# Performance work log

Hardware: AMD Instinct MI355X
Metric: run time of the kernel (lower is better)

## Reference

```python
import jax, jax.numpy as jnp
import numpy as np

N, K, D = 32768, 32, 64
LOG_2PI = float(np.log(2.0 * np.pi))


def setup_inputs() -> dict:
    key = jax.random.key(0)
    k1, k2, k3, k4 = jax.random.split(key, 4)
    X = jax.random.normal(k1, (N, D), dtype=jnp.float32)
    mu = jax.random.normal(k2, (K, D), dtype=jnp.float32)
    L = jax.random.normal(k3, (K, D, D), dtype=jnp.float32) * 0.1
    weights = jax.random.normal(k4, (K,), dtype=jnp.float32)
    return {"X": X, "mu": mu, "L": L, "weights": weights, "it": 0}


def reference(X, mu, L, weights, it):
    d = X.shape[1]
    # Cholesky composition: Sigma_k = tril(L_k) @ tril(L_k).T + I  (always PD)
    Lt = jnp.tril(L)                                   # [K, D, D]
    sigmas = Lt @ jnp.swapaxes(Lt, -1, -2) + jnp.eye(d, dtype=X.dtype)
    _, logdet = jnp.linalg.slogdet(sigmas)             # [K] (det > 0, sign = +1)
    Sinv = jnp.linalg.inv(sigmas)                      # [K, D, D]
    # Batched squared Mahalanobis distance: [N, K]
    diff = X[:, None, :] - mu[None, :, :]              # [N, K, D]
    maha = jnp.einsum("nkd,kde,nke->nk", diff, Sinv, diff)
    log_w = jax.nn.log_softmax(weights)                # [K]
    # log component density + log mixture weight
    logp = -0.5 * (d * LOG_2PI + logdet[None, :] + maha) + log_w[None, :]
    # pdf = sum_k exp(logp); log_likelihood = log(pdf)  (stable via logsumexp)
    loglik = jax.scipy.special.logsumexp(logp, axis=1)  # [N]
    # forward = -log_likelihoods(X).logsumexp(dim=0)
    return -jax.scipy.special.logsumexp(loglik, axis=0)
```

## Files before the change

kernel.cpp:

```cpp
#include <hip/hip_runtime.h>
#include <math.h>

#define DIM 64
#define KC 32
#define NPTS 32768
#define LOG_2PI 1.8378770664093453f
#define C0 (-58.0f)
#define ST 68

typedef __attribute__((ext_vector_type(8))) short short8;
typedef __attribute__((ext_vector_type(4))) float float4v;

__device__ __forceinline__ unsigned short f2bf(float f) {
    unsigned u = __float_as_uint(f);
    u += 0x7FFFu + ((u >> 16) & 1u);
    return (unsigned short)(u >> 16);
}

__device__ __forceinline__ float rdlane(float v, int l) {
    return __int_as_float(__builtin_amdgcn_readlane(__float_as_int(v), l));
}

__global__ __launch_bounds__(256) void conv_kernel(
    const float* __restrict__ X, short* __restrict__ Xbf)
{
    const int ctid = blockIdx.x * 256 + threadIdx.x;
    const float4* xin = (const float4*)X + (size_t)ctid * 2;
    float4 v0 = xin[0], v1 = xin[1];
    short8 o;
    o[0] = (short)f2bf(v0.x); o[1] = (short)f2bf(v0.y);
    o[2] = (short)f2bf(v0.z); o[3] = (short)f2bf(v0.w);
    o[4] = (short)f2bf(v1.x); o[5] = (short)f2bf(v1.y);
    o[6] = (short)f2bf(v1.z); o[7] = (short)f2bf(v1.w);
    *((short8*)Xbf + ctid) = o;
}

__global__ __launch_bounds__(256) void prep_kernel(
    const float* __restrict__ L, const float* __restrict__ mu,
    const float* __restrict__ w, short* __restrict__ Bpack,
    float* __restrict__ qpackN, float* __restrict__ cstC)
{
    const int k = blockIdx.x;
    const int t = threadIdx.x;
    const int wv = t >> 6;
    const int ln = t & 63;
    __shared__ float Llds[DIM * ST];
    __shared__ float Sig[DIM * ST];
    __shared__ float Clds[DIM * ST];
    __shared__ float Ylds[DIM * ST];
    __shared__ float rdbuf[DIM];

    for (int idx = t; idx < DIM * DIM; idx += 256) {
        int r = idx >> 6, c = idx & 63;
        float v = L[(size_t)k * DIM * DIM + idx];
        Llds[r * ST + c] = (c <= r) ? v : 0.f;
    }
    for (int idx = t; idx < DIM * ST; idx += 256) {
        Clds[idx] = 0.f;
        Ylds[idx] = 0.f;
    }
    __syncthreads();

    {
        float Lr[DIM];
        const float4* lp = (const float4*)(Llds + ln * ST);
#pragma unroll
        for (int p = 0; p < 16; ++p) {
            float4 v = lp[p];
            Lr[4 * p] = v.x; Lr[4 * p + 1] = v.y;
            Lr[4 * p + 2] = v.z; Lr[4 * p + 3] = v.w;
        }
#pragma unroll
        for (int jj = 0; jj < 16; ++jj) {
            const int j = jj * 4 + wv;
            const float4* up = (const float4*)(Llds + j * ST);
            const int pc = jj + 1;
            float a0 = 0.f, a1 = 0.f, a2 = 0.f, a3 = 0.f;
#pragma unroll
            for (int p = 0; p < pc; ++p) {
                float4 u = up[p];
                a0 = fmaf(Lr[4 * p], u.x, a0);
                a1 = fmaf(Lr[4 * p + 1], u.y, a1);
                a2 = fmaf(Lr[4 * p + 2], u.z, a2);
                a3 = fmaf(Lr[4 * p + 3], u.w, a3);
            }
            float s = (a0 + a1) + (a2 + a3);
            if (j == ln) s += 1.f;
            Sig[ln * ST + j] = s;
        }
    }
    __syncthreads();

    float ld2 = 0.f;
    {
        float Cr[DIM];
        float Yr[DIM];
#pragma unroll
        for (int c = 0; c < DIM; c += 8) {
            const float4* u0 = (const float4*)(Clds + (c + 0) * ST);
            const float4* u1 = (const float4*)(Clds + (c + 1) * ST);
            const float4* u2 = (const float4*)(Clds + (c + 2) * ST);
            const float4* u3 = (const float4*)(Clds + (c + 3) * ST);
            const float4* u4 = (const float4*)(Clds + (c + 4) * ST);
            const float4* u5 = (const float4*)(Clds + (c + 5) * ST);
            const float4* u6 = (const float4*)(Clds + (c + 6) * ST);
            const float4* u7 = (const float4*)(Clds + (c + 7) * ST);
            const int pc = c >> 2;
            float si0 = 0.f, si1 = 0.f, si2 = 0.f, si3 = 0.f;
            float si4 = 0.f, si5 = 0.f, si6 = 0.f, si7 = 0.f;
            if (wv == 0) {
                float d0a = 0.f, d0b = 0.f, d1a = 0.f, d1b = 0.f;
                float d2a = 0.f, d2b = 0.f, d3a = 0.f, d3b = 0.f;
                float d4a = 0.f, d4b = 0.f, d5a = 0.f, d5b = 0.f;
                float d6a = 0.f, d6b = 0.f, d7a = 0.f, d7b = 0.f;
#pragma unroll
                for (int p = 0; p < pc; ++p) {
                    float crx = Cr[4 * p], cry = Cr[4 * p + 1];
                    float crz = Cr[4 * p + 2], crw = Cr[4 * p + 3];
                    float4 q0 = u0[p], q1 = u1[p], q2 = u2[p], q3 = u3[p];
                    float4 q4 = u4[p], q5 = u5[p], q6 = u6[p], q7 = u7[p];
                    d0a = fmaf(crx, q0.x, d0a); d0b = fmaf(cry, q0.y, d0b);
                    d0a = fmaf(crz, q0.z, d0a); d0b = fmaf(crw, q0.w, d0b);
                    d1a = fmaf(crx, q1.x, d1a); d1b = fmaf(cry, q1.y, d1b);
                    d1a = fmaf(crz, q1.z, d1a); d1b = fmaf(crw, q1.w, d1b);
                    d2a = fmaf(crx, q2.x, d2a); d2b = fmaf(cry, q2.y, d2b);
                    d2a = fmaf(crz, q2.z, d2a); d2b = fmaf(crw, q2.w, d2b);
                    d3a = fmaf(crx, q3.x, d3a); d3b = fmaf(cry, q3.y, d3b);
                    d3a = fmaf(crz, q3.z, d3a); d3b = fmaf(crw, q3.w, d3b);
                    d4a = fmaf(crx, q4.x, d4a); d4b = fmaf(cry, q4.y, d4b);
                    d4a = fmaf(crz, q4.z, d4a); d4b = fmaf(crw, q4.w, d4b);
                    d5a = fmaf(crx, q5.x, d5a); d5b = fmaf(cry, q5.y, d5b);
                    d5a = fmaf(crz, q5.z, d5a); d5b = fmaf(crw, q5.w, d5b);
                    d6a = fmaf(crx, q6.x, d6a); d6b = fmaf(cry, q6.y, d6b);
                    d6a = fmaf(crz, q6.z, d6a); d6b = fmaf(crw, q6.w, d6b);
                    d7a = fmaf(crx, q7.x, d7a); d7b = fmaf(cry, q7.y, d7b);
                    d7a = fmaf(crz, q7.z, d7a); d7b = fmaf(crw, q7.w, d7b);
                }
                const float4 sgA = *(const float4*)(Sig + ln * ST + c);
                const float4 sgB = *(const float4*)(Sig + ln * ST + c + 4);
                float s0 = sgA.x - (d0a + d0b);
                float s1 = sgA.y - (d1a + d1b);
                float s2 = sgA.z - (d2a + d2b);
                float s3 = sgA.w - (d3a + d3b);
                float s4 = sgB.x - (d4a + d4b);
                float s5 = sgB.y - (d5a + d5b);
                float s6 = sgB.z - (d6a + d6b);
                float s7 = sgB.w - (d7a + d7b);
                float dd0 = rdlane(s0, c + 0);
                float rd0 = __builtin_amdgcn_rsqf(dd0);
                float c0v = s0 * rd0;
                s1 = fmaf(-c0v, rdlane(c0v, c + 1), s1);
                s2 = fmaf(-c0v, rdlane(c0v, c + 2), s2);
                s3 = fmaf(-c0v, rdlane(c0v, c + 3), s3);
                s4 = fmaf(-c0v, rdlane(c0v, c + 4), s4);
                s5 = fmaf(-c0v, rdlane(c0v, c + 5), s5);
                s6 = fmaf(-c0v, rdlane(c0v, c + 6), s6);
                s7 = fmaf(-c0v, rdlane(c0v, c + 7), s7);
                float dd1 = rdlane(s1, c + 1);
                float rd1 = __builtin_amdgcn_rsqf(dd1);
                float c1v = s1 * rd1;
                s2 = fmaf(-c1v, rdlane(c1v, c + 2), s2);
                s3 = fmaf(-c1v, rdlane(c1v, c + 3), s3);
                s4 = fmaf(-c1v, rdlane(c1v, c + 4), s4);
                s5 = fmaf(-c1v, rdlane(c1v, c + 5), s5);
                s6 = fmaf(-c1v, rdlane(c1v, c + 6), s6);
                s7 = fmaf(-c1v, rdlane(c1v, c + 7), s7);
                float dd2 = rdlane(s2, c + 2);
                float rd2 = __builtin_amdgcn_rsqf(dd2);
                float c2v = s2 * rd2;
                s3 = fmaf(-c2v, rdlane(c2v, c + 3), s3);
                s4 = fmaf(-c2v, rdlane(c2v, c + 4), s4);
                s5 = fmaf(-c2v, rdlane(c2v, c + 5), s5);
                s6 = fmaf(-c2v, rdlane(c2v, c + 6), s6);
                s7 = fmaf(-c2v, rdlane(c2v, c + 7), s7);
                float dd3 = rdlane(s3, c + 3);
                float rd3 = __builtin_amdgcn_rsqf(dd3);
                float c3v = s3 * rd3;
                s4 = fmaf(-c3v, rdlane(c3v, c + 4), s4);
                s5 = fmaf(-c3v, rdlane(c3v, c + 5), s5);
                s6 = fmaf(-c3v, rdlane(c3v, c + 6), s6);
                s7 = fmaf(-c3v, rdlane(c3v, c + 7), s7);
                float dd4 = rdlane(s4, c + 4);
                float rd4 = __builtin_amdgcn_rsqf(dd4);
                float c4v = s4 * rd4;
                s5 = fmaf(-c4v, rdlane(c4v, c + 5), s5);
                s6 = fmaf(-c4v, rdlane(c4v, c + 6), s6);
                s7 = fmaf(-c4v, rdlane(c4v, c + 7), s7);
                float dd5 = rdlane(s5, c + 5);
                float rd5 = __builtin_amdgcn_rsqf(dd5);
                float c5v = s5 * rd5;
                s6 = fmaf(-c5v, rdlane(c5v, c + 6), s6);
                s7 = fmaf(-c5v, rdlane(c5v, c + 7), s7);
                float dd6 = rdlane(s6, c + 6);
                float rd6 = __builtin_amdgcn_rsqf(dd6);
                float c6v = s6 * rd6;
                s7 = fmaf(-c6v, rdlane(c6v, c + 7), s7);
                float dd7 = rdlane(s7, c + 7);
                float rd7 = __builtin_amdgcn_rsqf(dd7);
                float c7v = s7 * rd7;
                ld2 += ((__logf(dd0) + __logf(dd1)) + (__logf(dd2) + __logf(dd3)))
                     + ((__logf(dd4) + __logf(dd5)) + (__logf(dd6) + __logf(dd7)));
                Cr[c + 0] = c0v; Cr[c + 1] = c1v; Cr[c + 2] = c2v; Cr[c + 3] = c3v;
                Cr[c + 4] = c4v; Cr[c + 5] = c5v; Cr[c + 6] = c6v; Cr[c + 7] = c7v;
                *(float4*)(Clds + ln * ST + c)     = make_float4(c0v, c1v, c2v, c3v);
                *(float4*)(Clds + ln * ST + c + 4) = make_float4(c4v, c5v, c6v, c7v);
                if (ln == 0) {
                    *(float4*)(rdbuf + c)     = make_float4(rd0, rd1, rd2, rd3);
                    *(float4*)(rdbuf + c + 4) = make_float4(rd4, rd5, rd6, rd7);
                }
            } else if (wv == 1) {
                float e0a = 0.f, e0b = 0.f, e1a = 0.f, e1b = 0.f;
                float e2a = 0.f, e2b = 0.f, e3a = 0.f, e3b = 0.f;
                float e4a = 0.f, e4b = 0.f, e5a = 0.f, e5b = 0.f;
                float e6a = 0.f, e6b = 0.f, e7a = 0.f, e7b = 0.f;
#pragma unroll
                for (int p = 0; p < pc; ++p) {
                    float yrx = Yr[4 * p], yry = Yr[4 * p + 1];
                    float yrz = Yr[4 * p + 2], yrw = Yr[4 * p + 3];
                    float4 q0 = u0[p], q1 = u1[p], q2 = u2[p], q3 = u3[p];
                    float4 q4 = u4[p], q5 = u5[p], q6 = u6[p], q7 = u7[p];
                    e0a = fmaf(yrx, q0.x, e0a); e0b = fmaf(yry, q0.y, e0b);
                    e0a = fmaf(yrz, q0.z, e0a); e0b = fmaf(yrw, q0.w, e0b);
                    e1a = fmaf(yrx, q1.x, e1a); e1b = fmaf(yry, q1.y, e1b);
                    e1a = fmaf(yrz, q1.z, e1a); e1b = fmaf(yrw, q1.w, e1b);
                    e2a = fmaf(yrx, q2.x, e2a); e2b = fmaf(yry, q2.y, e2b);
                    e2a = fmaf(yrz, q2.z, e2a); e2b = fmaf(yrw, q2.w, e2b);
                    e3a = fmaf(yrx, q3.x, e3a); e3b = fmaf(yry, q3.y, e3b);
                    e3a = fmaf(yrz, q3.z, e3a); e3b = fmaf(yrw, q3.w, e3b);
                    e4a = fmaf(yrx, q4.x, e4a); e4b = fmaf(yry, q4.y, e4b);
                    e4a = fmaf(yrz, q4.z, e4a); e4b = fmaf(yrw, q4.w, e4b);
                    e5a = fmaf(yrx, q5.x, e5a); e5b = fmaf(yry, q5.y, e5b);
                    e5a = fmaf(yrz, q5.z, e5a); e5b = fmaf(yrw, q5.w, e5b);
                    e6a = fmaf(yrx, q6.x, e6a); e6b = fmaf(yry, q6.y, e6b);
                    e6a = fmaf(yrz, q6.z, e6a); e6b = fmaf(yrw, q6.w, e6b);
                    e7a = fmaf(yrx, q7.x, e7a); e7b = fmaf(yry, q7.y, e7b);
                    e7a = fmaf(yrz, q7.z, e7a); e7b = fmaf(yrw, q7.w, e7b);
                }
                si0 = ((ln == c + 0) ? 1.f : 0.f) - (e0a + e0b);
                si1 = ((ln == c + 1) ? 1.f : 0.f) - (e1a + e1b);
                si2 = ((ln == c + 2) ? 1.f : 0.f) - (e2a + e2b);
                si3 = ((ln == c + 3) ? 1.f : 0.f) - (e3a + e3b);
                si4 = ((ln == c + 4) ? 1.f : 0.f) - (e4a + e4b);
                si5 = ((ln == c + 5) ? 1.f : 0.f) - (e5a + e5b);
                si6 = ((ln == c + 6) ? 1.f : 0.f) - (e6a + e6b);
                si7 = ((ln == c + 7) ? 1.f : 0.f) - (e7a + e7b);
            }
            __syncthreads();
            if (wv == 1) {
                const float4 rdv0 = *(const float4*)(rdbuf + c);
                const float4 rdv1 = *(const float4*)(rdbuf + c + 4);
                const float4 r1  = *(const float4*)(Clds + (c + 1) * ST + c);
                const float4 r2  = *(const float4*)(Clds + (c + 2) * ST + c);
                const float4 r3  = *(const float4*)(Clds + (c + 3) * ST + c);
                const float4 r4  = *(const float4*)(Clds + (c + 4) * ST + c);
                const float4 r5a = *(const float4*)(Clds + (c + 5) * ST + c);
                const float4 r5b = *(const float4*)(Clds + (c + 5) * ST + c + 4);
                const float4 r6a = *(const float4*)(Clds + (c + 6) * ST + c);
                const float4 r6b = *(const float4*)(Clds + (c + 6) * ST + c + 4);
                const float4 r7a = *(const float4*)(Clds + (c + 7) * ST + c);
                const float4 r7b = *(const float4*)(Clds + (c + 7) * ST + c + 4);
                float y0 = si0 * rdv0.x;
                float y1 = (si1 - r1.x * y0) * rdv0.y;
                float y2 = (si2 - r2.x * y0 - r2.y * y1) * rdv0.z;
                float y3 = (si3 - r3.x * y0 - r3.y * y1 - r3.z * y2) * rdv0.w;
                float y4 = (si4 - r4.x * y0 - r4.y * y1 - r4.z * y2 - r4.w * y3) * rdv1.x;
                float y5 = (si5 - r5a.x * y0 - r5a.y * y1 - r5a.z * y2 - r5a.w * y3
                                - r5b.x * y4) * rdv1.y;
                float y6 = (si6 - r6a.x * y0 - r6a.y * y1 - r6a.z * y2 - r6a.w * y3
                                - r6b.x * y4 - r6b.y * y5) * rdv1.z;
                float y7 = (si7 - r7a.x * y0 - r7a.y * y1 - r7a.z * y2 - r7a.w * y3
                                - r7b.x * y4 - r7b.y * y5 - r7b.z * y6) * rdv1.w;
                float4 yo0, yo1;
                yo0.x = (ln <= c + 0) ? y0 : 0.f;
                yo0.y = (ln <= c + 1) ? y1 : 0.f;
                yo0.z = (ln <= c + 2) ? y2 : 0.f;
                yo0.w = (ln <= c + 3) ? y3 : 0.f;
                yo1.x = (ln <= c + 4) ? y4 : 0.f;
                yo1.y = (ln <= c + 5) ? y5 : 0.f;
                yo1.z = (ln <= c + 6) ? y6 : 0.f;
                yo1.w = (ln <= c + 7) ? y7 : 0.f;
                Yr[c + 0] = yo0.x; Yr[c + 1] = yo0.y;
                Yr[c + 2] = yo0.z; Yr[c + 3] = yo0.w;
                Yr[c + 4] = yo1.x; Yr[c + 5] = yo1.y;
                Yr[c + 6] = yo1.z; Yr[c + 7] = yo1.w;
                *(float4*)(Ylds + ln * ST + c)     = yo0;
                *(float4*)(Ylds + ln * ST + c + 4) = yo1;
            }
        }
    }
    __syncthreads();

    if (wv == 0) {
        const float* muk = mu + k * DIM;
        float qv = 0.f;
#pragma unroll 8
        for (int j = 0; j < DIM; ++j)
            qv = fmaf(Ylds[j * ST + ln], muk[j], qv);
        qpackN[k * DIM + ln] = -qv;
        float wl = (ln < KC) ? w[ln] : -3.0e38f;
        float wm = wl;
#pragma unroll
        for (int m = 1; m <= 32; m <<= 1)
            wm = fmaxf(wm, __shfl_xor(wm, m, 64));
        float ex = (ln < KC) ? __expf(wl - wm) : 0.f;
#pragma unroll
        for (int m = 1; m <= 32; m <<= 1)
            ex += __shfl_xor(ex, m, 64);
        if (ln == 0) {
            float logw = w[k] - (wm + __logf(ex));
            cstC[k] = -0.5f * (DIM * LOG_2PI + ld2) + logw - C0;
        }
    }
    __syncthreads();

    {
        const int ct = wv;
        const int col = ct * 16 + (ln & 15);
        const int kb = (ln >> 4) * 8;
#pragma unroll
        for (int kt = 0; kt < 2; ++kt) {
            short8 v;
#pragma unroll
            for (int e = 0; e < 8; ++e)
                v[e] = (short)f2bf(Ylds[(kt * 32 + kb + e) * ST + col]);
            *(short8*)(Bpack + ((size_t)(k * 8 + ct * 2 + kt) * 64 + ln) * 8) = v;
        }
    }
}

__global__ __launch_bounds__(256, 4) void main_kernel(
    const short* __restrict__ Xbf, const float* __restrict__ Bpack,
    const float* __restrict__ qpackN, const float* __restrict__ cstC,
    float* __restrict__ partials)
{
    const int tid = threadIdx.x;
    const int lane = tid & 63;
    const int wv = tid >> 6;
    const int ks = blockIdx.x & 7;
    const int g = blockIdx.x >> 3;

    __shared__ float4 Bsh[2048];
    __shared__ float qsh[256];
    {
        const float4* Bg = (const float4*)Bpack + (size_t)ks * 2048;
#pragma unroll
        for (int it = 0; it < 8; ++it)
            Bsh[it * 256 + tid] = Bg[it * 256 + tid];
        qsh[tid] = qpackN[ks * 256 + tid];
    }

    const int rbase = g * 128 + wv * 32;
    const int jb = (lane >> 4) * 8;
    const int j8 = jb >> 3;
    const short8* xr = (const short8*)Xbf + (size_t)(rbase + (lane & 15)) * 8;
    short8 a0  = xr[j8];
    short8 a1  = xr[j8 + 4];
    short8 b0r = xr[j8 + 128];
    short8 b1r = xr[j8 + 132];

    __syncthreads();

    const short8* Bs = (const short8*)Bsh;
    float acc = 0.f;
#pragma unroll
    for (int kk = 0; kk < 4; ++kk) {
        const int k = ks * 4 + kk;
        float pA = 0.f, pB = 0.f;
#pragma unroll
        for (int ct = 0; ct < 4; ++ct) {
            short8 f0 = Bs[(kk * 8 + ct * 2 + 0) * 64 + lane];
            short8 f1 = Bs[(kk * 8 + ct * 2 + 1) * 64 + lane];
            const float4 nq4 = *(const float4*)(qsh + kk * 64 + ct * 16 + (lane >> 4) * 4);
            float4v c0 = {nq4.x, nq4.y, nq4.z, nq4.w};
            c0 = __builtin_amdgcn_mfma_f32_16x16x32_bf16(f0, a0, c0, 0, 0, 0);
            c0 = __builtin_amdgcn_mfma_f32_16x16x32_bf16(f1, a1, c0, 0, 0, 0);
            float4v c1 = {nq4.x, nq4.y, nq4.z, nq4.w};
            c1 = __builtin_amdgcn_mfma_f32_16x16x32_bf16(f0, b0r, c1, 0, 0, 0);
            c1 = __builtin_amdgcn_mfma_f32_16x16x32_bf16(f1, b1r, c1, 0, 0, 0);
            pA = fmaf(c0[0], c0[0], pA); pA = fmaf(c0[1], c0[1], pA);
            pA = fmaf(c0[2], c0[2], pA); pA = fmaf(c0[3], c0[3], pA);
            pB = fmaf(c1[0], c1[0], pB); pB = fmaf(c1[1], c1[1], pB);
            pB = fmaf(c1[2], c1[2], pB); pB = fmaf(c1[3], c1[3], pB);
        }
        pA += __shfl_xor(pA, 16, 64);
        pA += __shfl_xor(pA, 32, 64);
        pB += __shfl_xor(pB, 16, 64);
        pB += __shfl_xor(pB, 32, 64);
        const float cc = cstC[k];
        acc += __expf(fmaf(-0.5f, pA, cc)) + __expf(fmaf(-0.5f, pB, cc));
    }
    acc += __shfl_xor(acc, 1, 64);
    acc += __shfl_xor(acc, 2, 64);
    acc += __shfl_xor(acc, 4, 64);
    acc += __shfl_xor(acc, 8, 64);

    __shared__ float pm[4];
    if (lane == 0) pm[wv] = acc;
    __syncthreads();
    if (tid == 0)
        partials[blockIdx.x] = (pm[0] + pm[1]) + (pm[2] + pm[3]);
}

__global__ __launch_bounds__(256) void final_kernel(
    const float* __restrict__ partials, int n, float* __restrict__ out)
{
    const int tid = threadIdx.x;
    float s = 0.f;
    for (int i = tid; i < n; i += 256) s += partials[i];
#pragma unroll
    for (int m = 1; m <= 32; m <<= 1) s += __shfl_xor(s, m, 64);
    __shared__ float pm[4];
    if ((tid & 63) == 0) pm[tid >> 6] = s;
    __syncthreads();
    if (tid == 0) out[0] = -(C0 + logf((pm[0] + pm[1]) + (pm[2] + pm[3])));
}

extern "C" void kernel_launch(void* const* d_in, const int* in_sizes, int n_in,
                              void* d_out, int out_size, void* d_ws, size_t ws_size,
                              hipStream_t stream) {
    const float* X  = (const float*)d_in[0];
    const float* mu = (const float*)d_in[1];
    const float* L  = (const float*)d_in[2];
    const float* w  = (const float*)d_in[3];

    char* ws = (char*)d_ws;
    short* Bpack  = (short*)ws;
    float* qpackN = (float*)(ws + (256 << 10));
    float* cstC   = qpackN + KC * DIM;
    float* parts  = cstC + KC;
    short* Xbf    = (short*)(ws + (4 << 20));

    conv_kernel<<<1024, 256, 0, stream>>>(X, Xbf);
    prep_kernel<<<KC, 256, 0, stream>>>(L, mu, w, Bpack, qpackN, cstC);
    main_kernel<<<2048, 256, 0, stream>>>(Xbf, (const float*)Bpack, qpackN, cstC, parts);
    final_kernel<<<1, 256, 0, stream>>>(parts, 2048, (float*)d_out);
}
```

Measured before the change: 99.91 us.

## Fuse final reduction into main kernel via atomics and halve block count

Removes the separate final_kernel launch. Each main_kernel block now atomically adds its partial sum and increments a counter, and the last block to arrive computes the log and writes the output. The accumulator and counter are zeroed in conv_kernel. Each block also processes two row tiles, so the grid drops from 2048 to 1024 blocks and the B-tile LDS load is amortised over twice as many rows. The trade-off is a float atomic sum whose order varies between runs, so the result is non-deterministic, and fewer blocks means less parallelism.

```diff
diff --git a/kernel.cpp b/kernel.cpp
--- a/kernel.cpp
+++ b/kernel.cpp
@@ -22,8 +22,13 @@
 }
 
 __global__ __launch_bounds__(256) void conv_kernel(
-    const float* __restrict__ X, short* __restrict__ Xbf)
+    const float* __restrict__ X, short* __restrict__ Xbf,
+    float* __restrict__ accum, unsigned* __restrict__ counter)
 {
+    if (blockIdx.x == 0 && threadIdx.x == 0) {
+        *accum = 0.f;
+        *counter = 0u;
+    }
     const int ctid = blockIdx.x * 256 + threadIdx.x;
     const float4* xin = (const float4*)X + (size_t)ctid * 2;
     float4 v0 = xin[0], v1 = xin[1];
@@ -331,7 +336,8 @@
 __global__ __launch_bounds__(256, 4) void main_kernel(
     const short* __restrict__ Xbf, const float* __restrict__ Bpack,
     const float* __restrict__ qpackN, const float* __restrict__ cstC,
-    float* __restrict__ partials)
+    float* __restrict__ accum, unsigned* __restrict__ counter,
+    float* __restrict__ out)
 {
     const int tid = threadIdx.x;
     const int lane = tid & 63;
@@ -348,46 +354,47 @@
             Bsh[it * 256 + tid] = Bg[it * 256 + tid];
         qsh[tid] = qpackN[ks * 256 + tid];
     }
-
-    const int rbase = g * 128 + wv * 32;
-    const int jb = (lane >> 4) * 8;
-    const int j8 = jb >> 3;
-    const short8* xr = (const short8*)Xbf + (size_t)(rbase + (lane & 15)) * 8;
-    short8 a0  = xr[j8];
-    short8 a1  = xr[j8 + 4];
-    short8 b0r = xr[j8 + 128];
-    short8 b1r = xr[j8 + 132];
+    const int j8 = lane >> 4;
 
     __syncthreads();
 
     const short8* Bs = (const short8*)Bsh;
     float acc = 0.f;
-#pragma unroll
-    for (int kk = 0; kk < 4; ++kk) {
-        const int k = ks * 4 + kk;
-        float pA = 0.f, pB = 0.f;
-#pragma unroll
-        for (int ct = 0; ct < 4; ++ct) {
-            short8 f0 = Bs[(kk * 8 + ct * 2 + 0) * 64 + lane];
-            short8 f1 = Bs[(kk * 8 + ct * 2 + 1) * 64 + lane];
-            const float4 nq4 = *(const float4*)(qsh + kk * 64 + ct * 16 + (lane >> 4) * 4);
-            float4v c0 = {nq4.x, nq4.y, nq4.z, nq4.w};
-            c0 = __builtin_amdgcn_mfma_f32_16x16x32_bf16(f0, a0, c0, 0, 0, 0);
-            c0 = __builtin_amdgcn_mfma_f32_16x16x32_bf16(f1, a1, c0, 0, 0, 0);
-            float4v c1 = {nq4.x, nq4.y, nq4.z, nq4.w};
-            c1 = __builtin_amdgcn_mfma_f32_16x16x32_bf16(f0, b0r, c1, 0, 0, 0);
-            c1 = __builtin_amdgcn_mfma_f32_16x16x32_bf16(f1, b1r, c1, 0, 0, 0);
-            pA = fmaf(c0[0], c0[0], pA); pA = fmaf(c0[1], c0[1], pA);
-            pA = fmaf(c0[2], c0[2], pA); pA = fmaf(c0[3], c0[3], pA);
-            pB = fmaf(c1[0], c1[0], pB); pB = fmaf(c1[1], c1[1], pB);
-            pB = fmaf(c1[2], c1[2], pB); pB = fmaf(c1[3], c1[3], pB);
-        }
-        pA += __shfl_xor(pA, 16, 64);
-        pA += __shfl_xor(pA, 32, 64);
-        pB += __shfl_xor(pB, 16, 64);
-        pB += __shfl_xor(pB, 32, 64);
-        const float cc = cstC[k];
-        acc += __expf(fmaf(-0.5f, pA, cc)) + __expf(fmaf(-0.5f, pB, cc));
+#pragma unroll 1
+    for (int rr = 0; rr < 2; ++rr) {
+        const int rbase = g * 256 + rr * 128 + wv * 32;
+        const short8* xr = (const short8*)Xbf + (size_t)(rbase + (lane & 15)) * 8;
+        short8 a0  = xr[j8];
+        short8 a1  = xr[j8 + 4];
+        short8 b0r = xr[j8 + 128];
+        short8 b1r = xr[j8 + 132];
+#pragma unroll
+        for (int kk = 0; kk < 4; ++kk) {
+            const int k = ks * 4 + kk;
+            float pA = 0.f, pB = 0.f;
+#pragma unroll
+            for (int ct = 0; ct < 4; ++ct) {
+                short8 f0 = Bs[(kk * 8 + ct * 2 + 0) * 64 + lane];
+                short8 f1 = Bs[(kk * 8 + ct * 2 + 1) * 64 + lane];
+                const float4 nq4 = *(const float4*)(qsh + kk * 64 + ct * 16 + j8 * 4);
+                float4v c0 = {nq4.x, nq4.y, nq4.z, nq4.w};
+                c0 = __builtin_amdgcn_mfma_f32_16x16x32_bf16(f0, a0, c0, 0, 0, 0);
+                c0 = __builtin_amdgcn_mfma_f32_16x16x32_bf16(f1, a1, c0, 0, 0, 0);
+                float4v c1 = {nq4.x, nq4.y, nq4.z, nq4.w};
+                c1 = __builtin_amdgcn_mfma_f32_16x16x32_bf16(f0, b0r, c1, 0, 0, 0);
+                c1 = __builtin_amdgcn_mfma_f32_16x16x32_bf16(f1, b1r, c1, 0, 0, 0);
+                pA = fmaf(c0[0], c0[0], pA); pA = fmaf(c0[1], c0[1], pA);
+                pA = fmaf(c0[2], c0[2], pA); pA = fmaf(c0[3], c0[3], pA);
+                pB = fmaf(c1[0], c1[0], pB); pB = fmaf(c1[1], c1[1], pB);
+                pB = fmaf(c1[2], c1[2], pB); pB = fmaf(c1[3], c1[3], pB);
+            }
+            pA += __shfl_xor(pA, 16, 64);
+            pA += __shfl_xor(pA, 32, 64);
+            pB += __shfl_xor(pB, 16, 64);
+            pB += __shfl_xor(pB, 32, 64);
+            const float cc = cstC[k];
+            acc += __expf(fmaf(-0.5f, pA, cc)) + __expf(fmaf(-0.5f, pB, cc));
+        }
     }
     acc += __shfl_xor(acc, 1, 64);
     acc += __shfl_xor(acc, 2, 64);
@@ -397,22 +404,17 @@
     __shared__ float pm[4];
     if (lane == 0) pm[wv] = acc;
     __syncthreads();
-    if (tid == 0)
-        partials[blockIdx.x] = (pm[0] + pm[1]) + (pm[2] + pm[3]);
-}
-
-__global__ __launch_bounds__(256) void final_kernel(
-    const float* __restrict__ partials, int n, float* __restrict__ out)
-{
-    const int tid = threadIdx.x;
-    float s = 0.f;
-    for (int i = tid; i < n; i += 256) s += partials[i];
-#pragma unroll
-    for (int m = 1; m <= 32; m <<= 1) s += __shfl_xor(s, m, 64);
-    __shared__ float pm[4];
-    if ((tid & 63) == 0) pm[tid >> 6] = s;
-    __syncthreads();
-    if (tid == 0) out[0] = -(C0 + logf((pm[0] + pm[1]) + (pm[2] + pm[3])));
+    if (tid == 0) {
+        const float part = (pm[0] + pm[1]) + (pm[2] + pm[3]);
+        atomicAdd(accum, part);
+        __threadfence();
+        const unsigned old = atomicAdd(counter, 1u);
+        if (old == 1023u) {
+            __threadfence();
+            const float s = atomicAdd(accum, 0.f);
+            out[0] = -(C0 + __logf(s) );
+        }
+    }
 }
 
 extern "C" void kernel_launch(void* const* d_in, const int* in_sizes, int n_in,
@@ -427,11 +429,12 @@
     short* Bpack  = (short*)ws;
     float* qpackN = (float*)(ws + (256 << 10));
     float* cstC   = qpackN + KC * DIM;
-    float* parts  = cstC + KC;
+    float* accum  = cstC + KC;
+    unsigned* counter = (unsigned*)(accum + 1);
     short* Xbf    = (short*)(ws + (4 << 20));
 
-    conv_kernel<<<1024, 256, 0, stream>>>(X, Xbf);
+    conv_kernel<<<1024, 256, 0, stream>>>(X, Xbf, accum, counter);
     prep_kernel<<<KC, 256, 0, stream>>>(L, mu, w, Bpack, qpackN, cstC);
-    main_kernel<<<2048, 256, 0, stream>>>(Xbf, (const float*)Bpack, qpackN, cstC, parts);
-    final_kernel<<<1, 256, 0, stream>>>(parts, 2048, (float*)d_out);
-}
+    main_kernel<<<1024, 256, 0, stream>>>(Xbf, (const float*)Bpack, qpackN, cstC,
+                                          accum, counter, (float*)d_out);
+}
```

Measured after the change: 172.5 us. +72.6%, slower.

## Compute Sigma columns lazily inside the Cholesky loop on idle waves

Applied to the files above, without the earlier changes.

Instead of building the full Sigma = L L^T + I matrix before the factorisation, waves 2-3 compute only the first 8 columns up front. The remaining columns are then produced one 8-column panel ahead inside the Cholesky/inverse loop, while waves 0-1 do the panel work. This overlaps Sigma construction with the serial factorisation to shorten the per-component setup kernel. It relies on the existing barriers making each panel of Sigma ready before it is read, and keeps Lr live across the loop, which raises register pressure. The MFMA kernel also gets a trivial index simplification.

```diff
diff --git a/kernel.cpp b/kernel.cpp
--- a/kernel.cpp
+++ b/kernel.cpp
@@ -61,8 +61,8 @@
     }
     __syncthreads();
 
-    {
-        float Lr[DIM];
+    float Lr[DIM];
+    if (wv >= 2) {
         const float4* lp = (const float4*)(Llds + ln * ST);
 #pragma unroll
         for (int p = 0; p < 16; ++p) {
@@ -70,14 +70,14 @@
             Lr[4 * p] = v.x; Lr[4 * p + 1] = v.y;
             Lr[4 * p + 2] = v.z; Lr[4 * p + 3] = v.w;
         }
-#pragma unroll
-        for (int jj = 0; jj < 16; ++jj) {
-            const int j = jj * 4 + wv;
+        const int jbase = (wv - 2) * 4;
+#pragma unroll
+        for (int jj = 0; jj < 4; ++jj) {
+            const int j = jbase + jj;
             const float4* up = (const float4*)(Llds + j * ST);
-            const int pc = jj + 1;
             float a0 = 0.f, a1 = 0.f, a2 = 0.f, a3 = 0.f;
 #pragma unroll
-            for (int p = 0; p < pc; ++p) {
+            for (int p = 0; p < 2; ++p) {
                 float4 u = up[p];
                 a0 = fmaf(Lr[4 * p], u.x, a0);
                 a1 = fmaf(Lr[4 * p + 1], u.y, a1);
@@ -244,6 +244,27 @@
                 si5 = ((ln == c + 5) ? 1.f : 0.f) - (e5a + e5b);
                 si6 = ((ln == c + 6) ? 1.f : 0.f) - (e6a + e6b);
                 si7 = ((ln == c + 7) ? 1.f : 0.f) - (e7a + e7b);
+            } else if (c < DIM - 8) {
+                const int cb = c + 8;
+                const int jbase = cb + (wv - 2) * 4;
+                const int pcS = (cb >> 2) + 2;
+#pragma unroll
+                for (int jj = 0; jj < 4; ++jj) {
+                    const int j = jbase + jj;
+                    const float4* up = (const float4*)(Llds + j * ST);
+                    float a0 = 0.f, a1 = 0.f, a2 = 0.f, a3 = 0.f;
+#pragma unroll
+                    for (int p = 0; p < pcS; ++p) {
+                        float4 u = up[p];
+                        a0 = fmaf(Lr[4 * p], u.x, a0);
+                        a1 = fmaf(Lr[4 * p + 1], u.y, a1);
+                        a2 = fmaf(Lr[4 * p + 2], u.z, a2);
+                        a3 = fmaf(Lr[4 * p + 3], u.w, a3);
+                    }
+                    float s = (a0 + a1) + (a2 + a3);
+                    if (j == ln) s += 1.f;
+                    Sig[ln * ST + j] = s;
+                }
             }
             __syncthreads();
             if (wv == 1) {
@@ -350,8 +371,7 @@
     }
 
     const int rbase = g * 128 + wv * 32;
-    const int jb = (lane >> 4) * 8;
-    const int j8 = jb >> 3;
+    const int j8 = lane >> 4;
     const short8* xr = (const short8*)Xbf + (size_t)(rbase + (lane & 15)) * 8;
     short8 a0  = xr[j8];
     short8 a1  = xr[j8 + 4];
@@ -370,7 +390,7 @@
         for (int ct = 0; ct < 4; ++ct) {
             short8 f0 = Bs[(kk * 8 + ct * 2 + 0) * 64 + lane];
             short8 f1 = Bs[(kk * 8 + ct * 2 + 1) * 64 + lane];
-            const float4 nq4 = *(const float4*)(qsh + kk * 64 + ct * 16 + (lane >> 4) * 4);
+            const float4 nq4 = *(const float4*)(qsh + kk * 64 + ct * 16 + j8 * 4);
             float4v c0 = {nq4.x, nq4.y, nq4.z, nq4.w};
             c0 = __builtin_amdgcn_mfma_f32_16x16x32_bf16(f0, a0, c0, 0, 0, 0);
             c0 = __builtin_amdgcn_mfma_f32_16x16x32_bf16(f1, a1, c0, 0, 0, 0);
```

Result: no change. 99.68 us (-0.2%).
